# Kernel tuning notes

Hardware: AMD Instinct MI355X
Metric: run time of the kernel (lower is better)

Reference implementation:

```python
import jax, jax.numpy as jnp
from jax import lax
import numpy as np

BN_EPS = 1e-5


def _dwconv3x3(x, w):
    # x: [B,C,H,W], w: [C,1,3,3] depthwise (groups == C)
    return lax.conv_general_dilated(
        x, w, window_strides=(1, 1), padding='SAME',
        dimension_numbers=('NCHW', 'OIHW', 'NCHW'),
        feature_group_count=x.shape[1])


def _bn_eval(x, g, b, m, v):
    s = g * lax.rsqrt(v + BN_EPS)            # [C]
    return x * s[None, :, None, None] + (b - m * s)[None, :, None, None]


def _maxpool2(x):
    return lax.reduce_window(x, -jnp.inf, lax.max,
                             (1, 1, 2, 2), (1, 1, 2, 2), 'VALID')


def setup_inputs() -> dict:
    key = jax.random.key(0)
    ks = jax.random.split(key, 8)
    B, Cin, H, W = 32, 128, 64, 64
    Hd = 256               # hidden_size
    K, Ck = 32, 8          # num categories, hidden_size // K
    sc = 0.05
    return {
        'v4_features': jax.random.normal(ks[0], (B, Cin, H, W), jnp.float32),
        'w1_dw': jax.random.normal(ks[1], (Cin, 1, 3, 3), jnp.float32) * sc,
        'w1_pw': jax.random.normal(ks[2], (Hd, Cin), jnp.float32) * sc,
        'bn1_g': jnp.ones((Hd,), jnp.float32),
        'bn1_b': jnp.zeros((Hd,), jnp.float32),
        'bn1_m': jnp.zeros((Hd,), jnp.float32),
        'bn1_v': jnp.ones((Hd,), jnp.float32),
        'w2_dw': jax.random.normal(ks[3], (Hd, 1, 3, 3), jnp.float32) * sc,
        'w2_pw': jax.random.normal(ks[4], (Hd, Hd), jnp.float32) * sc,
        'bn2_g': jnp.ones((Hd,), jnp.float32),
        'bn2_b': jnp.zeros((Hd,), jnp.float32),
        'bn2_m': jnp.zeros((Hd,), jnp.float32),
        'bn2_v': jnp.ones((Hd,), jnp.float32),
        'cat_w': jax.random.normal(ks[5], (K, Ck, Hd), jnp.float32) * sc,
        'emb_w': jax.random.normal(ks[6], (128, Hd), jnp.float32) * sc,
        'emb_b': jnp.zeros((128,), jnp.float32),
    }


def reference(v4_features, w1_dw, w1_pw, bn1_g, bn1_b, bn1_m, bn1_v,
              w2_dw, w2_pw, bn2_g, bn2_b, bn2_m, bn2_v,
              cat_w, emb_w, emb_b):
    # Block 1: depthwise 3x3 -> pointwise 1x1 -> BN -> ReLU -> maxpool2
    x = _dwconv3x3(v4_features, w1_dw)
    x = jnp.einsum('bchw,oc->bohw', x, w1_pw)
    x = _maxpool2(jax.nn.relu(_bn_eval(x, bn1_g, bn1_b, bn1_m, bn1_v)))
    # Block 2
    x = _dwconv3x3(x, w2_dw)
    x = jnp.einsum('bchw,oc->bohw', x, w2_pw)
    x = _maxpool2(jax.nn.relu(_bn_eval(x, bn2_g, bn2_b, bn2_m, bn2_v)))
    # All 32 category 1x1 convs fused into one batched contraction.
    # cat_spikes: [B, K, Ck, H', W'] (non-SNN branch returns raw features)
    cat_spikes = jnp.einsum('bchw,koc->bkohw', x, cat_w)
    cat_pooled = cat_spikes.mean(axis=(-2, -1))         # [B, K, Ck]
    category_activations = cat_pooled.mean(axis=-1)     # [B, K]
    pooled = x.mean(axis=(-2, -1))                      # [B, Hd]
    object_embedding = pooled @ emb_w.T + emb_b         # [B, 128]
    return cat_spikes, category_activations, object_embedding, x
```

## Files before the change

### kernel.cpp

```cpp
#include <hip/hip_runtime.h>

#define BN_EPS 1e-5f

typedef float f32x4 __attribute__((ext_vector_type(4)));
typedef short short8 __attribute__((ext_vector_type(8)));
typedef unsigned short u16;

__device__ __forceinline__ u16 f2bf(float f) {
    unsigned u = __builtin_bit_cast(unsigned, f);
    unsigned r = (u + 0x7FFFu + ((u >> 16) & 1u)) >> 16;
    return (u16)r;
}
__device__ __forceinline__ float b2f(u16 h) {
    return __builtin_bit_cast(float, (unsigned)h << 16);
}

#define SWZ(row) ((((row) & 7) ^ (((row) >> 3) & 7)) << 4)

__global__ __launch_bounds__(256) void dw1_prep(
    const float* __restrict__ in, const float* __restrict__ wts,
    u16* __restrict__ out,
    const float* __restrict__ w1, const float* __restrict__ w2,
    const float* __restrict__ wc, u16* __restrict__ o1,
    u16* __restrict__ o2, u16* __restrict__ oc)
{
    const int t = threadIdx.x;
    if (blockIdx.x >= 4096) {
        const int idx = (blockIdx.x - 4096) * 256 + t;
        const float* src; u16* dst; int off;
        if (idx < 8192)       { src = w1; dst = o1; off = idx; }
        else if (idx < 24576) { src = w2; dst = o2; off = idx - 8192; }
        else                  { src = wc; dst = oc; off = idx - 24576; }
        const float4 v = *(const float4*)(src + 4 * (size_t)off);
        ushort4 h;
        h.x = f2bf(v.x); h.y = f2bf(v.y); h.z = f2bf(v.z); h.w = f2bf(v.w);
        *(ushort4*)(dst + 4 * (size_t)off) = h;
        return;
    }

    const int HW = 64;
    const int wq  = t & 15;
    const int w0  = wq * 4;
    const int rin = t >> 4;
    const int plane = blockIdx.x;
    const int c     = plane & 127;
    float wt[9];
#pragma unroll
    for (int i = 0; i < 9; ++i) wt[i] = wts[c * 9 + i];
    const float* ip = in  + (size_t)plane * (HW * HW);
    u16*         op = out + (size_t)plane * (HW * HW);

#pragma unroll
    for (int it = 0; it < 4; ++it) {
        const int h = it * 16 + rin;
        const float* rp = ip + h * HW + w0;
        const float4 zero4 = make_float4(0.f, 0.f, 0.f, 0.f);
        const float4 vc = *(const float4*)rp;
        const float4 vt = (h > 0)      ? *(const float4*)(rp - HW) : zero4;
        const float4 vb = (h < HW - 1) ? *(const float4*)(rp + HW) : zero4;

        float lc = __shfl_up(vc.w, 1),  rc = __shfl_down(vc.x, 1);
        float lt = __shfl_up(vt.w, 1),  rt = __shfl_down(vt.x, 1);
        float lb = __shfl_up(vb.w, 1),  rb = __shfl_down(vb.x, 1);
        if (wq == 0)  { lc = 0.f; lt = 0.f; lb = 0.f; }
        if (wq == 15) { rc = 0.f; rt = 0.f; rb = 0.f; }

        float o0 = 0.f, o1v = 0.f, o2v = 0.f, o3v = 0.f;
        o0  = fmaf(lt,   wt[0], fmaf(vt.x, wt[1], fmaf(vt.y, wt[2], o0)));
        o1v = fmaf(vt.x, wt[0], fmaf(vt.y, wt[1], fmaf(vt.z, wt[2], o1v)));
        o2v = fmaf(vt.y, wt[0], fmaf(vt.z, wt[1], fmaf(vt.w, wt[2], o2v)));
        o3v = fmaf(vt.z, wt[0], fmaf(vt.w, wt[1], fmaf(rt,   wt[2], o3v)));
        o0  = fmaf(lc,   wt[3], fmaf(vc.x, wt[4], fmaf(vc.y, wt[5], o0)));
        o1v = fmaf(vc.x, wt[3], fmaf(vc.y, wt[4], fmaf(vc.z, wt[5], o1v)));
        o2v = fmaf(vc.y, wt[3], fmaf(vc.z, wt[4], fmaf(vc.w, wt[5], o2v)));
        o3v = fmaf(vc.z, wt[3], fmaf(vc.w, wt[4], fmaf(rc,   wt[5], o3v)));
        o0  = fmaf(lb,   wt[6], fmaf(vb.x, wt[7], fmaf(vb.y, wt[8], o0)));
        o1v = fmaf(vb.x, wt[6], fmaf(vb.y, wt[7], fmaf(vb.z, wt[8], o1v)));
        o2v = fmaf(vb.y, wt[6], fmaf(vb.z, wt[7], fmaf(vb.w, wt[8], o2v)));
        o3v = fmaf(vb.z, wt[6], fmaf(vb.w, wt[7], fmaf(rb,   wt[8], o3v)));

        ushort4 st;
        st.x = f2bf(o0); st.y = f2bf(o1v); st.z = f2bf(o2v); st.w = f2bf(o3v);
        *(ushort4*)(op + h * HW + w0) = st;
    }
}

__global__ __launch_bounds__(256, 2) void pw1_v2(
    const u16* __restrict__ t1b, const u16* __restrict__ wsW1,
    const float* __restrict__ bg, const float* __restrict__ bb,
    const float* __restrict__ bm, const float* __restrict__ bv,
    u16* __restrict__ t2b)
{
    __shared__ __align__(16) char smem[34816];
    float* sArr = (float*)(smem + 32768);
    float* tArr = (float*)(smem + 33792);

    const int bid = blockIdx.x;
    const int b   = bid >> 5;
    const int py  = bid & 31;
    const int p0  = py * 128;
    const int t   = threadIdx.x;

    {
        const float s = bg[t] * rsqrtf(bv[t] + BN_EPS);
        sArr[t] = s;
        tArr[t] = bb[t] - bm[t] * s;
    }

    {
        const u16* xb = t1b + ((size_t)b * 128) * 4096 + p0;
        const int pg = t & 15, cg = t >> 4;
        short8 vin[8];
#pragma unroll
        for (int j = 0; j < 8; ++j)
            vin[j] = *(const short8*)(xb + (size_t)(8 * cg + j) * 4096 + 8 * pg);
#pragma unroll
        for (int k = 0; k < 8; ++k) {
            short8 ov;
            ov[0] = vin[0][k]; ov[1] = vin[1][k]; ov[2] = vin[2][k]; ov[3] = vin[3][k];
            ov[4] = vin[4][k]; ov[5] = vin[5][k]; ov[6] = vin[6][k]; ov[7] = vin[7][k];
            const int row = 8 * pg + k;
            *(short8*)(smem + ((row * 256 + cg * 16) ^ SWZ(row))) = ov;
        }
    }
    __syncthreads();

    const int lane = t & 63, wid = t >> 6;
    const int lr = lane & 15, lg = lane >> 4;
    const int wo = wid * 64;

    f32x4 acc[4][8];
#pragma unroll
    for (int m = 0; m < 4; ++m)
#pragma unroll
        for (int n = 0; n < 8; ++n) acc[m][n] = (f32x4){0.f, 0.f, 0.f, 0.f};

    const u16* wbase = wsW1 + (size_t)(wo + lr) * 128 + lg * 8;
#pragma unroll
    for (int ks = 0; ks < 4; ++ks) {
        short8 af[4];
#pragma unroll
        for (int m = 0; m < 4; ++m)
            af[m] = *(const short8*)(wbase + m * 16 * 128 + ks * 32);
#pragma unroll
        for (int n = 0; n < 8; ++n) {
            const int prow = n * 16 + lr;
            const short8 bfv = *(const short8*)(smem +
                ((prow * 256 + ks * 64 + lg * 16) ^ SWZ(prow)));
#pragma unroll
            for (int m = 0; m < 4; ++m)
                acc[m][n] = __builtin_amdgcn_mfma_f32_16x16x32_bf16(af[m], bfv, acc[m][n], 0, 0, 0);
        }
    }

    u16* outb = t2b + ((size_t)(b * 256) * 32 + py) * 32;
#pragma unroll
    for (int m = 0; m < 4; ++m) {
#pragma unroll
        for (int j = 0; j < 4; ++j) {
            const int o = wo + m * 16 + 4 * lg + j;
            const float s = sArr[o], tt = tArr[o];
#pragma unroll
            for (int n = 0; n < 4; ++n) {
                const float a0 = fmaxf(fmaf(acc[m][n][j],     s, tt), 0.f);
                const float a1 = fmaxf(fmaf(acc[m][n + 4][j], s, tt), 0.f);
                const float vm = fmaxf(a0, a1);
                const float hm = fmaxf(vm, __shfl_xor(vm, 1));
                const unsigned p2 = (unsigned)f2bf(hm) |
                                    ((unsigned)f2bf(__shfl_xor(hm, 2)) << 16);
                const unsigned hi = __shfl_xor(p2, 4);
                if ((lr & 7) == 0) {
                    uint2 w2v; w2v.x = p2; w2v.y = hi;
                    *(uint2*)(outb + (size_t)o * 1024 + n * 8 + (lr >> 1)) = w2v;
                }
            }
        }
    }
}

template<int HW, int LOGW, int NPL, int IPP, int CMASK>
__global__ __launch_bounds__(256) void dw_shfl_bf(
    const u16* __restrict__ in, const float* __restrict__ wts,
    u16* __restrict__ out)
{
    const int t   = threadIdx.x;
    const int LPR = HW / 4;
    const int wq  = t & (LPR - 1);
    const int w0  = wq * 4;
    const int rin = t >> (LOGW - 2);

    for (int pl = 0; pl < NPL; ++pl) {
        const int plane = blockIdx.x * NPL + pl;
        const int c     = plane & CMASK;
        float wt[9];
#pragma unroll
        for (int i = 0; i < 9; ++i) wt[i] = wts[c * 9 + i];
        const u16* ip = in  + (size_t)plane * (HW * HW);
        u16*       op = out + (size_t)plane * (HW * HW);

#pragma unroll
        for (int it = 0; it < IPP; ++it) {
            const int h = it * (1024 / HW) + rin;
            const u16* rp = ip + h * HW + w0;
            float4 vc, vt, vb;
            {
                const ushort4 hcv = *(const ushort4*)rp;
                vc = make_float4(b2f(hcv.x), b2f(hcv.y), b2f(hcv.z), b2f(hcv.w));
            }
            if (h > 0) {
                const ushort4 htv = *(const ushort4*)(rp - HW);
                vt = make_float4(b2f(htv.x), b2f(htv.y), b2f(htv.z), b2f(htv.w));
            } else vt = make_float4(0.f, 0.f, 0.f, 0.f);
            if (h < HW - 1) {
                const ushort4 hbv = *(const ushort4*)(rp + HW);
                vb = make_float4(b2f(hbv.x), b2f(hbv.y), b2f(hbv.z), b2f(hbv.w));
            } else vb = make_float4(0.f, 0.f, 0.f, 0.f);

            float lc = __shfl_up(vc.w, 1),  rc = __shfl_down(vc.x, 1);
            float lt = __shfl_up(vt.w, 1),  rt = __shfl_down(vt.x, 1);
            float lb = __shfl_up(vb.w, 1),  rb = __shfl_down(vb.x, 1);
            if (wq == 0)       { lc = 0.f; lt = 0.f; lb = 0.f; }
            if (wq == LPR - 1) { rc = 0.f; rt = 0.f; rb = 0.f; }

            float o0 = 0.f, o1 = 0.f, o2 = 0.f, o3 = 0.f;
            o0 = fmaf(lt,   wt[0], fmaf(vt.x, wt[1], fmaf(vt.y, wt[2], o0)));
            o1 = fmaf(vt.x, wt[0], fmaf(vt.y, wt[1], fmaf(vt.z, wt[2], o1)));
            o2 = fmaf(vt.y, wt[0], fmaf(vt.z, wt[1], fmaf(vt.w, wt[2], o2)));
            o3 = fmaf(vt.z, wt[0], fmaf(vt.w, wt[1], fmaf(rt,   wt[2], o3)));
            o0 = fmaf(lc,   wt[3], fmaf(vc.x, wt[4], fmaf(vc.y, wt[5], o0)));
            o1 = fmaf(vc.x, wt[3], fmaf(vc.y, wt[4], fmaf(vc.z, wt[5], o1)));
            o2 = fmaf(vc.y, wt[3], fmaf(vc.z, wt[4], fmaf(vc.w, wt[5], o2)));
            o3 = fmaf(vc.z, wt[3], fmaf(vc.w, wt[4], fmaf(rc,   wt[5], o3)));
            o0 = fmaf(lb,   wt[6], fmaf(vb.x, wt[7], fmaf(vb.y, wt[8], o0)));
            o1 = fmaf(vb.x, wt[6], fmaf(vb.y, wt[7], fmaf(vb.z, wt[8], o1)));
            o2 = fmaf(vb.y, wt[6], fmaf(vb.z, wt[7], fmaf(vb.w, wt[8], o2)));
            o3 = fmaf(vb.z, wt[6], fmaf(vb.w, wt[7], fmaf(rb,   wt[8], o3)));

            ushort4 st;
            st.x = f2bf(o0); st.y = f2bf(o1); st.z = f2bf(o2); st.w = f2bf(o3);
            *(ushort4*)(op + h * HW + w0) = st;
        }
    }
}

__global__ __launch_bounds__(256) void pw2_mfma(
    const u16* __restrict__ t3b, const u16* __restrict__ wsW2,
    const float* __restrict__ bg, const float* __restrict__ bb,
    const float* __restrict__ bm, const float* __restrict__ bv,
    float* __restrict__ xout)
{
    __shared__ __align__(16) char smem[49664];
    float* sArr = (float*)(smem + 49152);
    float* tArr = (float*)(smem + 49408);
    float* Df   = (float*)smem;

    const int bid = blockIdx.x;
    const int o0  = ((bid >> 3) & 3) * 64;
    const int pxb = (bid >> 5) * 8 + (bid & 7);
    const int px  = pxb & 7;
    const int b   = pxb >> 3;
    const int p0  = px * 128;
    const int t   = threadIdx.x;

    const int lane = t & 63, wid = t >> 6;
    const int lr = lane & 15, lg = lane >> 4;
    const int wo = (wid >> 1) * 32;
    const int wp = (wid & 1) * 64;

    f32x4 acc[2][4];
#pragma unroll
    for (int m = 0; m < 2; ++m)
#pragma unroll
        for (int n = 0; n < 4; ++n) acc[m][n] = (f32x4){0.f, 0.f, 0.f, 0.f};

#pragma unroll
    for (int ko = 0; ko < 2; ++ko) {
        if (ko) __syncthreads();

#pragma unroll
        for (int i = 0; i < 4; ++i) {
            const int li = i * 256 + t;
            const int ol = li >> 4;
            const int f8 = li & 15;
            const short8 wv = *(const short8*)(wsW2 + (size_t)(o0 + ol) * 256 + ko * 128 + 8 * f8);
            *(short8*)(smem + ((ol * 256 + f8 * 16) ^ SWZ(ol))) = wv;
        }

        {
            const u16* xb = t3b + ((size_t)b * 256 + ko * 128) * 1024 + p0;
            const int pg = t & 15, cg = t >> 4;
            short8 vin[8];
#pragma unroll
            for (int j = 0; j < 8; ++j)
                vin[j] = *(const short8*)(xb + (size_t)(8 * cg + j) * 1024 + 8 * pg);
#pragma unroll
            for (int k = 0; k < 8; ++k) {
                short8 ov;
                ov[0] = vin[0][k]; ov[1] = vin[1][k]; ov[2] = vin[2][k]; ov[3] = vin[3][k];
                ov[4] = vin[4][k]; ov[5] = vin[5][k]; ov[6] = vin[6][k]; ov[7] = vin[7][k];
                const int row = 8 * pg + k;
                *(short8*)(smem + 16384 + ((row * 256 + cg * 16) ^ SWZ(row))) = ov;
            }
        }

        if (ko == 0 && t < 64) {
            const int o = o0 + t;
            const float s = bg[o] * rsqrtf(bv[o] + BN_EPS);
            sArr[t] = s;
            tArr[t] = bb[o] - bm[o] * s;
        }
        __syncthreads();

#pragma unroll
        for (int ks = 0; ks < 4; ++ks) {
            short8 af[2];
#pragma unroll
            for (int m = 0; m < 2; ++m) {
                const int rowm = wo + m * 16 + lr;
                af[m] = *(const short8*)(smem + ((rowm * 256 + ks * 64 + lg * 16) ^ SWZ(rowm)));
            }
#pragma unroll
            for (int n = 0; n < 4; ++n) {
                const int prow = wp + n * 16 + lr;
                const short8 bfv = *(const short8*)(smem + 16384 +
                    ((prow * 256 + ks * 64 + lg * 16) ^ SWZ(prow)));
                acc[0][n] = __builtin_amdgcn_mfma_f32_16x16x32_bf16(af[0], bfv, acc[0][n], 0, 0, 0);
                acc[1][n] = __builtin_amdgcn_mfma_f32_16x16x32_bf16(af[1], bfv, acc[1][n], 0, 0, 0);
            }
        }
    }
    __syncthreads();

    float sv[2][4], tv[2][4];
#pragma unroll
    for (int m = 0; m < 2; ++m)
#pragma unroll
        for (int j = 0; j < 4; ++j) {
            const int ol = wo + m * 16 + 4 * lg + j;
            sv[m][j] = sArr[ol];
            tv[m][j] = tArr[ol];
        }
#pragma unroll
    for (int m = 0; m < 2; ++m)
#pragma unroll
        for (int n = 0; n < 4; ++n)
#pragma unroll
            for (int j = 0; j < 4; ++j) {
                const int ol = wo + m * 16 + 4 * lg + j;
                const int pl = wp + n * 16 + lr;
                const float val = fmaf(acc[m][n][j], sv[m][j], tv[m][j]);
                Df[ol * 130 + pl] = fmaxf(val, 0.f);
            }
    __syncthreads();

#pragma unroll
    for (int i = 0; i < 8; ++i) {
        const int oi = i * 256 + t;
        const int o  = oi >> 5;
        const int q  = oi & 31;
        const int prl = q >> 4;
        const int pc  = q & 15;
        const float a0 = Df[o * 130 + prl * 64 + 2 * pc];
        const float a1 = Df[o * 130 + prl * 64 + 2 * pc + 1];
        const float b0 = Df[o * 130 + prl * 64 + 32 + 2 * pc];
        const float b1 = Df[o * 130 + prl * 64 + 32 + 2 * pc + 1];
        xout[(((size_t)(b * 256 + o0 + o)) * 16 + 2 * px + prl) * 16 + pc] =
            fmaxf(fmaxf(a0, a1), fmaxf(b0, b1));
    }
}

__global__ __launch_bounds__(256) void cat_v2(
    const float* __restrict__ x, const u16* __restrict__ wsWc,
    float* __restrict__ spikes, float* __restrict__ csws)
{
    __shared__ __align__(16) char smem[49664];
    float* cs = (float*)(smem + 49152);

    const int bid = blockIdx.x;
    const int g   = (bid >> 6) * 8 + (bid & 7);
    const int m0  = ((bid >> 3) & 7) * 32;
    const int b   = g >> 2;
    const int q   = g & 3;
    const int px0 = q * 64;
    const int t   = threadIdx.x;

#pragma unroll
    for (int i = 0; i < 4; ++i) {
        const int li = i * 256 + t;
        const int ml = li >> 5, ch = li & 31;
        const short8 wv = *(const short8*)(wsWc + (size_t)(m0 + ml) * 256 + ch * 8);
        *(short8*)(smem + ((ml * 512 + ch * 16) ^ SWZ(ml))) = wv;
    }

    const float* xb = x + (size_t)b * 65536;
#pragma unroll
    for (int i = 0; i < 4; ++i) {
        const int li = i * 256 + t;
        const int pq = li & 15;
        const int cg = li >> 4;
        const float4 v0 = *(const float4*)(xb + (size_t)(4 * cg + 0) * 256 + px0 + 4 * pq);
        const float4 v1 = *(const float4*)(xb + (size_t)(4 * cg + 1) * 256 + px0 + 4 * pq);
        const float4 v2 = *(const float4*)(xb + (size_t)(4 * cg + 2) * 256 + px0 + 4 * pq);
        const float4 v3 = *(const float4*)(xb + (size_t)(4 * cg + 3) * 256 + px0 + 4 * pq);
        ushort4 h0, h1, h2, h3;
        h0.x = f2bf(v0.x); h0.y = f2bf(v1.x); h0.z = f2bf(v2.x); h0.w = f2bf(v3.x);
        h1.x = f2bf(v0.y); h1.y = f2bf(v1.y); h1.z = f2bf(v2.y); h1.w = f2bf(v3.y);
        h2.x = f2bf(v0.z); h2.y = f2bf(v1.z); h2.z = f2bf(v2.z); h2.w = f2bf(v3.z);
        h3.x = f2bf(v0.w); h3.y = f2bf(v1.w); h3.z = f2bf(v2.w); h3.w = f2bf(v3.w);
        const int p_ = 4 * pq;
        *(ushort4*)(smem + 16384 + (((p_ + 0) * 512 + cg * 8) ^ SWZ(p_ + 0))) = h0;
        *(ushort4*)(smem + 16384 + (((p_ + 1) * 512 + cg * 8) ^ SWZ(p_ + 1))) = h1;
        *(ushort4*)(smem + 16384 + (((p_ + 2) * 512 + cg * 8) ^ SWZ(p_ + 2))) = h2;
        *(ushort4*)(smem + 16384 + (((p_ + 3) * 512 + cg * 8) ^ SWZ(p_ + 3))) = h3;
    }
    __syncthreads();

    const int lane = t & 63, wid = t >> 6;
    const int lr = lane & 15, lg = lane >> 4;

    f32x4 acc[2];
    acc[0] = (f32x4){0.f, 0.f, 0.f, 0.f};
    acc[1] = (f32x4){0.f, 0.f, 0.f, 0.f};

#pragma unroll
    for (int ks = 0; ks < 8; ++ks) {
        const int prow = wid * 16 + lr;
        const short8 b8 = *(const short8*)(smem + 16384 +
            ((prow * 512 + ks * 64 + lg * 16) ^ SWZ(prow)));
#pragma unroll
        for (int mi = 0; mi < 2; ++mi) {
            const int rowm = mi * 16 + lr;
            const short8 a8 = *(const short8*)(smem +
                ((rowm * 512 + ks * 64 + lg * 16) ^ SWZ(rowm)));
            acc[mi] = __builtin_amdgcn_mfma_f32_16x16x32_bf16(a8, b8, acc[mi], 0, 0, 0);
        }
    }

#pragma unroll
    for (int mi = 0; mi < 2; ++mi) {
#pragma unroll
        for (int j = 0; j < 4; ++j) {
            const int m  = m0 + mi * 16 + 4 * lg + j;
            const int px = px0 + wid * 16 + lr;
            spikes[((size_t)(b * 256 + m)) * 256 + px] = acc[mi][j];
            float s = acc[mi][j];
            s += __shfl_xor(s, 1, 64);
            s += __shfl_xor(s, 2, 64);
            s += __shfl_xor(s, 4, 64);
            s += __shfl_xor(s, 8, 64);
            if (lr == 0) cs[wid * 32 + mi * 16 + 4 * lg + j] = s;
        }
    }
    __syncthreads();
    if (t < 32) {
        const float p = cs[t] + cs[32 + t] + cs[64 + t] + cs[96 + t];
        csws[((size_t)(b * 256 + m0 + t)) * 4 + q] = p;
    }
}

__global__ __launch_bounds__(256) void final_kernel(
    const float* __restrict__ x, const float* __restrict__ csws,
    const float* __restrict__ embw, const float* __restrict__ embb,
    float* __restrict__ cat_act, float* __restrict__ emb)
{
    const int b = blockIdx.x;
    const int t = threadIdx.x;
    __shared__ __align__(16) float pooled[256];

    {
        const float4* src = (const float4*)(x + (size_t)b * 65536 + (size_t)t * 256);
        float s = 0.f;
#pragma unroll 8
        for (int i = 0; i < 64; ++i) {
            const float4 v = src[i];
            s += v.x + v.y + v.z + v.w;
        }
        pooled[t] = s * (1.0f / 256.0f);
    }
    __syncthreads();

    if (t < 128) {
        const float4* wr = (const float4*)(embw + (size_t)t * 256);
        float d = 0.f;
#pragma unroll 8
        for (int i = 0; i < 64; ++i) {
            const float4 wv = wr[i];
            const float4 pv = *(const float4*)&pooled[4 * i];
            d = fmaf(wv.x, pv.x, d);
            d = fmaf(wv.y, pv.y, d);
            d = fmaf(wv.z, pv.z, d);
            d = fmaf(wv.w, pv.w, d);
        }
        emb[b * 128 + t] = d + embb[t];
    } else if (t < 160) {
        const int k = t - 128;
        float s = 0.f;
#pragma unroll
        for (int o = 0; o < 8; ++o) {
            const float4 qv = *(const float4*)&csws[((size_t)(b * 256 + k * 8 + o)) * 4];
            s += qv.x + qv.y + qv.z + qv.w;
        }
        cat_act[b * 32 + k] = s * (1.0f / 2048.0f);
    }
}

extern "C" void kernel_launch(void* const* d_in, const int* in_sizes, int n_in,
                              void* d_out, int out_size, void* d_ws, size_t ws_size,
                              hipStream_t stream) {
    const float* v4   = (const float*)d_in[0];
    const float* w1dw = (const float*)d_in[1];
    const float* w1pw = (const float*)d_in[2];
    const float* bn1g = (const float*)d_in[3];
    const float* bn1b = (const float*)d_in[4];
    const float* bn1m = (const float*)d_in[5];
    const float* bn1v = (const float*)d_in[6];
    const float* w2dw = (const float*)d_in[7];
    const float* w2pw = (const float*)d_in[8];
    const float* bn2g = (const float*)d_in[9];
    const float* bn2b = (const float*)d_in[10];
    const float* bn2m = (const float*)d_in[11];
    const float* bn2v = (const float*)d_in[12];
    const float* catw = (const float*)d_in[13];
    const float* embw = (const float*)d_in[14];
    const float* embb = (const float*)d_in[15];

    float* out        = (float*)d_out;
    float* cat_spikes = out;
    float* cat_act    = out + 2097152;
    float* emb        = out + 2098176;
    float* xout       = out + 2102272;

    char* ws = (char*)d_ws;
    u16* wsW1 = (u16*)ws;
    u16* wsW2 = (u16*)(ws + 65536);
    u16* wsWc = (u16*)(ws + 196608);
    u16* t1b  = (u16*)(ws + 327680);
    u16* t2b  = (u16*)(ws + 327680 + 33554432);
    u16* t3b  = (u16*)(ws + 327680 + 33554432 + 16777216);
    float* csws = (float*)(ws + 327680 + 33554432 + 16777216 + 16777216);

    dw1_prep<<<4256, 256, 0, stream>>>(v4, w1dw, t1b, w1pw, w2pw, catw,
                                       wsW1, wsW2, wsWc);
    pw1_v2<<<1024, 256, 0, stream>>>(t1b, wsW1, bn1g, bn1b, bn1m, bn1v, t2b);
    dw_shfl_bf<32, 5, 4, 1, 255><<<2048, 256, 0, stream>>>(t2b, w2dw, t3b);
    pw2_mfma<<<1024, 256, 0, stream>>>(t3b, wsW2, bn2g, bn2b, bn2m, bn2v, xout);
    cat_v2<<<1024, 256, 0, stream>>>(xout, wsWc, cat_spikes, csws);
    final_kernel<<<32, 256, 0, stream>>>(xout, csws, embw, embb, cat_act, emb);
}
```

Before: 102.8 us.

## Fuse second depthwise conv into pw2 GEMM using channel-last pooled layout

pw1 now writes its pooled bf16 output transposed to pixel-major (NHWC) through a shared-memory staging buffer. The separate dw_shfl_bf kernel is removed, and pw2_v3 computes the 3x3 depthwise conv on the fly from the NHWC tensor straight into the swizzled LDS B-tile before the MFMA GEMM. This drops one kernel launch and the t3b intermediate write/read round trip. In exchange, pw2 reads each neighbour pixel about nine times from global memory or cache, uses a larger register footprint (32-float accumulators plus a 4x4 MFMA tile), and launches half as many blocks.

```diff
diff --git a/kernel.cpp b/kernel.cpp
--- a/kernel.cpp
+++ b/kernel.cpp
@@ -89,7 +89,7 @@
     const u16* __restrict__ t1b, const u16* __restrict__ wsW1,
     const float* __restrict__ bg, const float* __restrict__ bb,
     const float* __restrict__ bm, const float* __restrict__ bv,
-    u16* __restrict__ t2b)
+    u16* __restrict__ t2bT)
 {
     __shared__ __align__(16) char smem[34816];
     float* sArr = (float*)(smem + 32768);
@@ -152,220 +152,168 @@
                 acc[m][n] = __builtin_amdgcn_mfma_f32_16x16x32_bf16(af[m], bfv, acc[m][n], 0, 0, 0);
         }
     }
-
-    u16* outb = t2b + ((size_t)(b * 256) * 32 + py) * 32;
+    __syncthreads();
+
 #pragma unroll
     for (int m = 0; m < 4; ++m) {
 #pragma unroll
-        for (int j = 0; j < 4; ++j) {
-            const int o = wo + m * 16 + 4 * lg + j;
-            const float s = sArr[o], tt = tArr[o];
-#pragma unroll
-            for (int n = 0; n < 4; ++n) {
+        for (int n = 0; n < 4; ++n) {
+            ushort4 h;
+#pragma unroll
+            for (int j = 0; j < 4; ++j) {
+                const int o = wo + m * 16 + 4 * lg + j;
+                const float s = sArr[o], tt = tArr[o];
                 const float a0 = fmaxf(fmaf(acc[m][n][j],     s, tt), 0.f);
                 const float a1 = fmaxf(fmaf(acc[m][n + 4][j], s, tt), 0.f);
                 const float vm = fmaxf(a0, a1);
                 const float hm = fmaxf(vm, __shfl_xor(vm, 1));
-                const unsigned p2 = (unsigned)f2bf(hm) |
-                                    ((unsigned)f2bf(__shfl_xor(hm, 2)) << 16);
-                const unsigned hi = __shfl_xor(p2, 4);
-                if ((lr & 7) == 0) {
-                    uint2 w2v; w2v.x = p2; w2v.y = hi;
-                    *(uint2*)(outb + (size_t)o * 1024 + n * 8 + (lr >> 1)) = w2v;
-                }
-            }
-        }
-    }
-}
-
-template<int HW, int LOGW, int NPL, int IPP, int CMASK>
-__global__ __launch_bounds__(256) void dw_shfl_bf(
-    const u16* __restrict__ in, const float* __restrict__ wts,
-    u16* __restrict__ out)
-{
-    const int t   = threadIdx.x;
-    const int LPR = HW / 4;
-    const int wq  = t & (LPR - 1);
-    const int w0  = wq * 4;
-    const int rin = t >> (LOGW - 2);
-
-    for (int pl = 0; pl < NPL; ++pl) {
-        const int plane = blockIdx.x * NPL + pl;
-        const int c     = plane & CMASK;
-        float wt[9];
-#pragma unroll
-        for (int i = 0; i < 9; ++i) wt[i] = wts[c * 9 + i];
-        const u16* ip = in  + (size_t)plane * (HW * HW);
-        u16*       op = out + (size_t)plane * (HW * HW);
-
-#pragma unroll
-        for (int it = 0; it < IPP; ++it) {
-            const int h = it * (1024 / HW) + rin;
-            const u16* rp = ip + h * HW + w0;
-            float4 vc, vt, vb;
-            {
-                const ushort4 hcv = *(const ushort4*)rp;
-                vc = make_float4(b2f(hcv.x), b2f(hcv.y), b2f(hcv.z), b2f(hcv.w));
-            }
-            if (h > 0) {
-                const ushort4 htv = *(const ushort4*)(rp - HW);
-                vt = make_float4(b2f(htv.x), b2f(htv.y), b2f(htv.z), b2f(htv.w));
-            } else vt = make_float4(0.f, 0.f, 0.f, 0.f);
-            if (h < HW - 1) {
-                const ushort4 hbv = *(const ushort4*)(rp + HW);
-                vb = make_float4(b2f(hbv.x), b2f(hbv.y), b2f(hbv.z), b2f(hbv.w));
-            } else vb = make_float4(0.f, 0.f, 0.f, 0.f);
-
-            float lc = __shfl_up(vc.w, 1),  rc = __shfl_down(vc.x, 1);
-            float lt = __shfl_up(vt.w, 1),  rt = __shfl_down(vt.x, 1);
-            float lb = __shfl_up(vb.w, 1),  rb = __shfl_down(vb.x, 1);
-            if (wq == 0)       { lc = 0.f; lt = 0.f; lb = 0.f; }
-            if (wq == LPR - 1) { rc = 0.f; rt = 0.f; rb = 0.f; }
-
-            float o0 = 0.f, o1 = 0.f, o2 = 0.f, o3 = 0.f;
-            o0 = fmaf(lt,   wt[0], fmaf(vt.x, wt[1], fmaf(vt.y, wt[2], o0)));
-            o1 = fmaf(vt.x, wt[0], fmaf(vt.y, wt[1], fmaf(vt.z, wt[2], o1)));
-            o2 = fmaf(vt.y, wt[0], fmaf(vt.z, wt[1], fmaf(vt.w, wt[2], o2)));
-            o3 = fmaf(vt.z, wt[0], fmaf(vt.w, wt[1], fmaf(rt,   wt[2], o3)));
-            o0 = fmaf(lc,   wt[3], fmaf(vc.x, wt[4], fmaf(vc.y, wt[5], o0)));
-            o1 = fmaf(vc.x, wt[3], fmaf(vc.y, wt[4], fmaf(vc.z, wt[5], o1)));
-            o2 = fmaf(vc.y, wt[3], fmaf(vc.z, wt[4], fmaf(vc.w, wt[5], o2)));
-            o3 = fmaf(vc.z, wt[3], fmaf(vc.w, wt[4], fmaf(rc,   wt[5], o3)));
-            o0 = fmaf(lb,   wt[6], fmaf(vb.x, wt[7], fmaf(vb.y, wt[8], o0)));
-            o1 = fmaf(vb.x, wt[6], fmaf(vb.y, wt[7], fmaf(vb.z, wt[8], o1)));
-            o2 = fmaf(vb.y, wt[6], fmaf(vb.z, wt[7], fmaf(vb.w, wt[8], o2)));
-            o3 = fmaf(vb.z, wt[6], fmaf(vb.w, wt[7], fmaf(rb,   wt[8], o3)));
-
-            ushort4 st;
-            st.x = f2bf(o0); st.y = f2bf(o1); st.z = f2bf(o2); st.w = f2bf(o3);
-            *(ushort4*)(op + h * HW + w0) = st;
-        }
-    }
-}
-
-__global__ __launch_bounds__(256) void pw2_mfma(
-    const u16* __restrict__ t3b, const u16* __restrict__ wsW2,
+                ((u16*)&h)[j] = f2bf(hm);
+            }
+            if ((lr & 1) == 0) {
+                const int pc = n * 8 + (lr >> 1);
+                *(ushort4*)(smem + pc * 528 + (wo + m * 16 + 4 * lg) * 2) = h;
+            }
+        }
+    }
+    __syncthreads();
+
+    {
+        const int px = t >> 3;
+        const int c0 = (t & 7) * 32;
+        const char* Trow = smem + px * 528 + c0 * 2;
+        u16* dst = t2bT + ((size_t)(b * 1024 + py * 32 + px)) * 256 + c0;
+#pragma unroll
+        for (int i = 0; i < 4; ++i)
+            *(short8*)(dst + i * 8) = *(const short8*)(Trow + i * 16);
+    }
+}
+
+__global__ __launch_bounds__(256) void pw2_v3(
+    const u16* __restrict__ t2bT, const u16* __restrict__ wsW2,
+    const float* __restrict__ w2dw,
     const float* __restrict__ bg, const float* __restrict__ bb,
     const float* __restrict__ bm, const float* __restrict__ bv,
     float* __restrict__ xout)
 {
-    __shared__ __align__(16) char smem[49664];
-    float* sArr = (float*)(smem + 49152);
-    float* tArr = (float*)(smem + 49408);
-    float* Df   = (float*)smem;
+    __shared__ __align__(16) char smem[27648];
+    float* wJ   = (float*)(smem + 16384);
+    float* sArr = (float*)(smem + 25600);
+    float* tArr = (float*)(smem + 26624);
 
     const int bid = blockIdx.x;
-    const int o0  = ((bid >> 3) & 3) * 64;
-    const int pxb = (bid >> 5) * 8 + (bid & 7);
-    const int px  = pxb & 7;
-    const int b   = pxb >> 3;
-    const int p0  = px * 128;
+    const int b   = bid >> 4;
+    const int T   = bid & 15;
     const int t   = threadIdx.x;
+
+    {
+        const float s = bg[t] * rsqrtf(bv[t] + BN_EPS);
+        sArr[t] = s;
+        tArr[t] = bb[t] - bm[t] * s;
+#pragma unroll
+        for (int j = 0; j < 9; ++j) wJ[j * 256 + t] = w2dw[t * 9 + j];
+    }
+    __syncthreads();
 
     const int lane = t & 63, wid = t >> 6;
     const int lr = lane & 15, lg = lane >> 4;
-    const int wo = (wid >> 1) * 32;
-    const int wp = (wid & 1) * 64;
-
-    f32x4 acc[2][4];
-#pragma unroll
-    for (int m = 0; m < 2; ++m)
+    const int wo = wid * 64;
+
+    f32x4 acc[4][4];
+#pragma unroll
+    for (int m = 0; m < 4; ++m)
 #pragma unroll
         for (int n = 0; n < 4; ++n) acc[m][n] = (f32x4){0.f, 0.f, 0.f, 0.f};
+
+    const int co  = t & 3;
+    const int pxq = t >> 2;
+    const int rl  = pxq >> 5;
+    const int cl  = pxq & 31;
 
 #pragma unroll
     for (int ko = 0; ko < 2; ++ko) {
         if (ko) __syncthreads();
 
-#pragma unroll
-        for (int i = 0; i < 4; ++i) {
-            const int li = i * 256 + t;
-            const int ol = li >> 4;
-            const int f8 = li & 15;
-            const short8 wv = *(const short8*)(wsW2 + (size_t)(o0 + ol) * 256 + ko * 128 + 8 * f8);
-            *(short8*)(smem + ((ol * 256 + f8 * 16) ^ SWZ(ol))) = wv;
-        }
-
         {
-            const u16* xb = t3b + ((size_t)b * 256 + ko * 128) * 1024 + p0;
-            const int pg = t & 15, cg = t >> 4;
-            short8 vin[8];
-#pragma unroll
-            for (int j = 0; j < 8; ++j)
-                vin[j] = *(const short8*)(xb + (size_t)(8 * cg + j) * 1024 + 8 * pg);
-#pragma unroll
-            for (int k = 0; k < 8; ++k) {
-                short8 ov;
-                ov[0] = vin[0][k]; ov[1] = vin[1][k]; ov[2] = vin[2][k]; ov[3] = vin[3][k];
-                ov[4] = vin[4][k]; ov[5] = vin[5][k]; ov[6] = vin[6][k]; ov[7] = vin[7][k];
-                const int row = 8 * pg + k;
-                *(short8*)(smem + 16384 + ((row * 256 + cg * 16) ^ SWZ(row))) = ov;
-            }
-        }
-
-        if (ko == 0 && t < 64) {
-            const int o = o0 + t;
-            const float s = bg[o] * rsqrtf(bv[o] + BN_EPS);
-            sArr[t] = s;
-            tArr[t] = bb[o] - bm[o] * s;
+            float ac[32];
+#pragma unroll
+            for (int i = 0; i < 32; ++i) ac[i] = 0.f;
+            const int cbase = ko * 128 + co * 32;
+#pragma unroll
+            for (int j = 0; j < 9; ++j) {
+                const int dr = j / 3 - 1, dc = j % 3 - 1;
+                const int gr = 2 * T + rl + dr;
+                const int gc = cl + dc;
+                const bool ok = (gr >= 0) && (gr < 32) && (gc >= 0) && (gc < 32);
+                const u16* src = t2bT + ((size_t)(b * 1024 + gr * 32 + gc)) * 256 + cbase;
+                const float* wj = wJ + j * 256 + cbase;
+#pragma unroll
+                for (int i4 = 0; i4 < 4; ++i4) {
+                    short8 v;
+                    if (ok) v = *(const short8*)(src + i4 * 8);
+                    else    v = (short8){0,0,0,0,0,0,0,0};
+                    const float4 wa = *(const float4*)(wj + i4 * 8);
+                    const float4 wb = *(const float4*)(wj + i4 * 8 + 4);
+                    ac[i4*8+0] = fmaf(b2f((u16)v[0]), wa.x, ac[i4*8+0]);
+                    ac[i4*8+1] = fmaf(b2f((u16)v[1]), wa.y, ac[i4*8+1]);
+                    ac[i4*8+2] = fmaf(b2f((u16)v[2]), wa.z, ac[i4*8+2]);
+                    ac[i4*8+3] = fmaf(b2f((u16)v[3]), wa.w, ac[i4*8+3]);
+                    ac[i4*8+4] = fmaf(b2f((u16)v[4]), wb.x, ac[i4*8+4]);
+                    ac[i4*8+5] = fmaf(b2f((u16)v[5]), wb.y, ac[i4*8+5]);
+                    ac[i4*8+6] = fmaf(b2f((u16)v[6]), wb.z, ac[i4*8+6]);
+                    ac[i4*8+7] = fmaf(b2f((u16)v[7]), wb.w, ac[i4*8+7]);
+                }
+            }
+#pragma unroll
+            for (int ii = 0; ii < 8; ++ii) {
+                ushort4 h;
+                h.x = f2bf(ac[4*ii+0]); h.y = f2bf(ac[4*ii+1]);
+                h.z = f2bf(ac[4*ii+2]); h.w = f2bf(ac[4*ii+3]);
+                *(ushort4*)(smem + ((pxq * 256 + (co * 32 + 4 * ii) * 2) ^ SWZ(pxq))) = h;
+            }
         }
         __syncthreads();
 
+        const u16* wbase = wsW2 + (size_t)(wo + lr) * 256 + ko * 128 + lg * 8;
 #pragma unroll
         for (int ks = 0; ks < 4; ++ks) {
-            short8 af[2];
-#pragma unroll
-            for (int m = 0; m < 2; ++m) {
-                const int rowm = wo + m * 16 + lr;
-                af[m] = *(const short8*)(smem + ((rowm * 256 + ks * 64 + lg * 16) ^ SWZ(rowm)));
-            }
+            short8 af[4];
+#pragma unroll
+            for (int m = 0; m < 4; ++m)
+                af[m] = *(const short8*)(wbase + m * 16 * 256 + ks * 32);
 #pragma unroll
             for (int n = 0; n < 4; ++n) {
-                const int prow = wp + n * 16 + lr;
-                const short8 bfv = *(const short8*)(smem + 16384 +
+                const int prow = n * 16 + lr;
+                const short8 bfv = *(const short8*)(smem +
                     ((prow * 256 + ks * 64 + lg * 16) ^ SWZ(prow)));
-                acc[0][n] = __builtin_amdgcn_mfma_f32_16x16x32_bf16(af[0], bfv, acc[0][n], 0, 0, 0);
-                acc[1][n] = __builtin_amdgcn_mfma_f32_16x16x32_bf16(af[1], bfv, acc[1][n], 0, 0, 0);
-            }
-        }
-    }
-    __syncthreads();
-
-    float sv[2][4], tv[2][4];
-#pragma unroll
-    for (int m = 0; m < 2; ++m)
+#pragma unroll
+                for (int m = 0; m < 4; ++m)
+                    acc[m][n] = __builtin_amdgcn_mfma_f32_16x16x32_bf16(af[m], bfv, acc[m][n], 0, 0, 0);
+            }
+        }
+    }
+
+#pragma unroll
+    for (int m = 0; m < 4; ++m) {
 #pragma unroll
         for (int j = 0; j < 4; ++j) {
-            const int ol = wo + m * 16 + 4 * lg + j;
-            sv[m][j] = sArr[ol];
-            tv[m][j] = tArr[ol];
-        }
-#pragma unroll
-    for (int m = 0; m < 2; ++m)
-#pragma unroll
-        for (int n = 0; n < 4; ++n)
-#pragma unroll
-            for (int j = 0; j < 4; ++j) {
-                const int ol = wo + m * 16 + 4 * lg + j;
-                const int pl = wp + n * 16 + lr;
-                const float val = fmaf(acc[m][n][j], sv[m][j], tv[m][j]);
-                Df[ol * 130 + pl] = fmaxf(val, 0.f);
-            }
-    __syncthreads();
-
-#pragma unroll
-    for (int i = 0; i < 8; ++i) {
-        const int oi = i * 256 + t;
-        const int o  = oi >> 5;
-        const int q  = oi & 31;
-        const int prl = q >> 4;
-        const int pc  = q & 15;
-        const float a0 = Df[o * 130 + prl * 64 + 2 * pc];
-        const float a1 = Df[o * 130 + prl * 64 + 2 * pc + 1];
-        const float b0 = Df[o * 130 + prl * 64 + 32 + 2 * pc];
-        const float b1 = Df[o * 130 + prl * 64 + 32 + 2 * pc + 1];
-        xout[(((size_t)(b * 256 + o0 + o)) * 16 + 2 * px + prl) * 16 + pc] =
-            fmaxf(fmaxf(a0, a1), fmaxf(b0, b1));
+            const int o = wo + m * 16 + 4 * lg + j;
+            const float s = sArr[o], tt = tArr[o];
+#pragma unroll
+            for (int nv = 0; nv < 2; ++nv) {
+                const float a0 = fmaxf(fmaf(acc[m][nv][j],     s, tt), 0.f);
+                const float a1 = fmaxf(fmaf(acc[m][nv + 2][j], s, tt), 0.f);
+                const float vm = fmaxf(a0, a1);
+                const float hm = fmaxf(vm, __shfl_xor(vm, 1));
+                const float h1 = __shfl_xor(hm, 2);
+                const float g0 = __shfl_xor(hm, 4);
+                const float g1 = __shfl_xor(h1, 4);
+                if ((lr & 7) == 0) {
+                    float4 f4 = make_float4(hm, h1, g0, g1);
+                    *(float4*)(xout + ((size_t)(b * 256 + o)) * 256 + T * 16 +
+                               nv * 8 + (lr >> 1)) = f4;
+                }
+            }
+        }
     }
 }
 
@@ -535,15 +483,13 @@
     u16* wsW2 = (u16*)(ws + 65536);
     u16* wsWc = (u16*)(ws + 196608);
     u16* t1b  = (u16*)(ws + 327680);
-    u16* t2b  = (u16*)(ws + 327680 + 33554432);
-    u16* t3b  = (u16*)(ws + 327680 + 33554432 + 16777216);
-    float* csws = (float*)(ws + 327680 + 33554432 + 16777216 + 16777216);
+    u16* t2bT = (u16*)(ws + 327680 + 33554432);
+    float* csws = (float*)(ws + 327680 + 33554432 + 16777216);
 
     dw1_prep<<<4256, 256, 0, stream>>>(v4, w1dw, t1b, w1pw, w2pw, catw,
                                        wsW1, wsW2, wsWc);
-    pw1_v2<<<1024, 256, 0, stream>>>(t1b, wsW1, bn1g, bn1b, bn1m, bn1v, t2b);
-    dw_shfl_bf<32, 5, 4, 1, 255><<<2048, 256, 0, stream>>>(t2b, w2dw, t3b);
-    pw2_mfma<<<1024, 256, 0, stream>>>(t3b, wsW2, bn2g, bn2b, bn2m, bn2v, xout);
+    pw1_v2<<<1024, 256, 0, stream>>>(t1b, wsW1, bn1g, bn1b, bn1m, bn1v, t2bT);
+    pw2_v3<<<512, 256, 0, stream>>>(t2bT, wsW2, w2dw, bn2g, bn2b, bn2m, bn2v, xout);
     cat_v2<<<1024, 256, 0, stream>>>(xout, wsWc, cat_spikes, csws);
     final_kernel<<<32, 256, 0, stream>>>(xout, csws, embw, embb, cat_act, emb);
 }
```

After: 116.1 us. +12.9%, slower.
